# Kernel optimization log

Hardware: AMD Instinct MI355X
Metric: run time of the kernel (lower is better)

The kernel has to match this reference:

```python
import jax, jax.numpy as jnp
import numpy as np

FMAP = 5
C = 2048
NC = 201  # n_classes + 1


def _conv(x, w, stride, pad):
    return jax.lax.conv_general_dilated(
        x, w, (stride, stride), [(pad, pad), (pad, pad)],
        dimension_numbers=('NCHW', 'OIHW', 'NCHW'))


def _bn(x, g, b, eps=1e-5):
    # training-mode batch norm (batch statistics), as in the torch forward
    m = x.mean((0, 2, 3), keepdims=True)
    v = x.var((0, 2, 3), keepdims=True)
    return (x - m) / jnp.sqrt(v + eps) * g[None, :, None, None] + b[None, :, None, None]


def _grid_sample(img, grid):
    # img [B,C,H,W]; grid [B,K,2] normalized coords (x,y), align_corners=True,
    # bilinear, zero padding -> [B,C,K]
    B, Ch, H, W = img.shape
    gx = (grid[..., 0] + 1.0) * 0.5 * (W - 1)
    gy = (grid[..., 1] + 1.0) * 0.5 * (H - 1)
    x0 = jnp.floor(gx); y0 = jnp.floor(gy)
    x1 = x0 + 1.0; y1 = y0 + 1.0
    wx1 = gx - x0; wx0 = 1.0 - wx1
    wy1 = gy - y0; wy0 = 1.0 - wy1
    imgf = img.reshape(B, Ch, H * W)

    def gather(xi, yi):
        valid = (xi >= 0) & (xi <= W - 1) & (yi >= 0) & (yi <= H - 1)
        xi_ = jnp.clip(xi, 0, W - 1).astype(jnp.int32)
        yi_ = jnp.clip(yi, 0, H - 1).astype(jnp.int32)
        idx = yi_ * W + xi_  # [B,K]
        v = jnp.take_along_axis(imgf, idx[:, None, :], axis=2)  # [B,C,K]
        return v * valid[:, None, :].astype(img.dtype)

    out = (gather(x0, y0) * (wx0 * wy0)[:, None, :]
           + gather(x1, y0) * (wx1 * wy0)[:, None, :]
           + gather(x0, y1) * (wx0 * wy1)[:, None, :]
           + gather(x1, y1) * (wx1 * wy1)[:, None, :])
    return out


def setup_inputs() -> dict:
    key = jax.random.key(0)
    ks = jax.random.split(key, 12)
    B = 8
    return {
        'x': jax.random.normal(ks[0], (B, C, 10, 10), jnp.float32),
        'epoch': 1,
        'flag': 0,
        'conv_last_w': jax.random.normal(ks[1], (C, C, 3, 3), jnp.float32) * 0.02,
        'bn_last_g': jnp.ones((C,), jnp.float32),
        'bn_last_b': jnp.zeros((C,), jnp.float32),
        'loc_w1': jax.random.normal(ks[2], (C, C, 3, 3), jnp.float32) * 0.02,
        'loc_g1': jnp.ones((C,), jnp.float32),
        'loc_b1': jnp.zeros((C,), jnp.float32),
        'loc_w2': jax.random.normal(ks[3], (C, C, 3, 3), jnp.float32) * 0.02,
        'loc_g2': jnp.ones((C,), jnp.float32),
        'loc_b2': jnp.zeros((C,), jnp.float32),
        'fc1_w': jax.random.normal(ks[4], (512, C * 9), jnp.float32) * 0.02,
        'fc2_w': jax.random.normal(ks[5], (4, 512), jnp.float32) * 0.001,
        'conv_stn_w': jax.random.normal(ks[6], (NC, C, 3, 3), jnp.float32) * 0.02,
        'conv_stn_b': jnp.zeros((NC,), jnp.float32),
    }


def reference(x, epoch, flag, conv_last_w, bn_last_g, bn_last_b,
              loc_w1, loc_g1, loc_b1, loc_w2, loc_g2, loc_b2,
              fc1_w, fc2_w, conv_stn_w, conv_stn_b):
    B = x.shape[0]
    # backbone tail: conv_last (s=2, pad=1) + bn_last -> [B,2048,5,5]
    f = _bn(_conv(x, conv_last_w, 2, 1), bn_last_g, bn_last_b)

    # localization network (conv-bn-relu x2, pad=1) -> [B,2048,5,5]
    xs = jax.nn.relu(_bn(_conv(f, loc_w1, 1, 1), loc_g1, loc_b1))
    xs = jax.nn.relu(_bn(_conv(xs, loc_w2, 1, 1), loc_g2, loc_b2))
    xs_p = jnp.pad(xs, ((0, 0), (0, 0), (1, 1), (1, 1)))  # [B,2048,7,7]

    # batched per-cell fc_loc: 25 overlapping 3x3 patches (i outer, j inner)
    patches = jnp.stack([xs_p[:, :, i:i + 3, j:j + 3]
                         for i in range(FMAP) for j in range(FMAP)], axis=1)
    patches = patches.reshape(B, FMAP * FMAP, C * 9)  # (C, kh, kw) flatten order
    h = jax.nn.relu(jnp.einsum('bpf,hf->bph', patches, fc1_w))
    p = jnp.einsum('bph,oh->bpo', h, fc2_w)  # [B,25,4]

    # theta = [[1+p0, 0, p1], [0, 1+p2, p3]]
    zero = jnp.zeros_like(p[..., 0])
    row0 = jnp.stack([1.0 + p[..., 0], zero, p[..., 1]], -1)
    row1 = jnp.stack([zero, 1.0 + p[..., 2], p[..., 3]], -1)
    theta = jnp.stack([row0, row1], -2)  # [B,25,2,3]

    # identity affine grid on padded 7x7 map (align_corners=True), 3x3 windows
    lin = jnp.linspace(-1.0, 1.0, FMAP + 2)
    gxm, gym = jnp.meshgrid(lin, lin, indexing='xy')  # gxm[y,x]=lin[x]
    base = jnp.stack([gxm, gym], -1)  # [7,7,2]
    pos = jnp.stack([base[i:i + 3, j:j + 3]
                     for i in range(FMAP) for j in range(FMAP)], 0)
    pos_h = jnp.concatenate([pos.reshape(25, 9, 2), jnp.ones((25, 9, 1))], -1)

    # transformed sampling grids: pos_hom @ theta^T -> [B,25,9,2]
    grids = jnp.einsum('pkc,bpdc->bpkd', pos_h, theta).reshape(B, 25 * 9, 2)

    # batched grid_sample of padded features, then stitch 25 3x3 tiles -> 15x15
    f_p = jnp.pad(f, ((0, 0), (0, 0), (1, 1), (1, 1)))  # [B,2048,7,7]
    samp = _grid_sample(f_p, grids)  # [B,C,225]
    temp = samp.reshape(B, C, FMAP, FMAP, 3, 3).transpose(0, 1, 2, 4, 3, 5)
    temp = temp.reshape(B, C, 3 * FMAP, 3 * FMAP)  # [B,2048,15,15]

    # conv_stn (k=3, s=3) -> [B,201,5,5]; joint softmax over class x position
    out = _conv(temp, conv_stn_w, 3, 0) + conv_stn_b[None, :, None, None]
    s = jax.nn.softmax(out.reshape(B, -1), axis=1).reshape(B, NC, FMAP, FMAP)
    classif_scores = s.sum((2, 3))  # [B,201]
    return classif_scores, s, theta.reshape(B * 25, 2, 3)
```

## Files before the change

kernel.cpp:

```cpp
#include <hip/hip_runtime.h>
#include <hip/hip_bf16.h>


#define GK 18432
#define GN 200
#define NPAD 256

typedef __attribute__((ext_vector_type(8))) short bf16x8;
typedef __attribute__((ext_vector_type(4))) float f32x4;
typedef unsigned int u32;

__global__ __launch_bounds__(256) void im2col_bf16(
    const float* __restrict__ in, __hip_bfloat16* __restrict__ Bt,
    int H, int stride, int pad)
{
    int tid = blockIdx.x * 256 + threadIdx.x;
    int n = tid / GK;
    int k = tid - n * GK;
    float v = 0.f;
    if (n < GN) {
        int c = k / 9; int r9 = k - c * 9;
        int kh = r9 / 3, kw = r9 - kh * 3;
        int b = n / 25; int pp = n - b * 25;
        int oh = pp / 5, ow = pp - oh * 5;
        int r = oh * stride + kh - pad;
        int s = ow * stride + kw - pad;
        if (r >= 0 && r < H && s >= 0 && s < H)
            v = in[(((b * 2048 + c) * H) + r) * H + s];
    }
    Bt[tid] = __float2bfloat16(v);
}

__global__ __launch_bounds__(256) void gridsample_bf16(
    const float* __restrict__ f, const float* __restrict__ gridb,
    __hip_bfloat16* __restrict__ Bt)
{
    int tid = blockIdx.x * 256 + threadIdx.x;
    int n = tid / GK;
    int cq = tid - n * GK;
    float v = 0.f;
    if (n < GN) {
        int c = cq / 9, q = cq - c * 9;
        int b = n / 25, p = n - b * 25;
        int g = (b * 225 + p * 9 + q) * 2;
        float px = gridb[g], py = gridb[g + 1];
        float x0f = floorf(px), y0f = floorf(py);
        int x0 = (int)x0f, y0 = (int)y0f;
        float wx1 = px - x0f, wx0 = 1.f - wx1;
        float wy1 = py - y0f, wy0 = 1.f - wy1;
        const float* fb = f + ((size_t)b * 2048 + c) * 25;
        auto fetch = [&](int xi, int yi) -> float {
            if (xi < 1 || xi > 5 || yi < 1 || yi > 5) return 0.f;
            return fb[(yi - 1) * 5 + (xi - 1)];
        };
        v = fetch(x0, y0) * wx0 * wy0
          + fetch(x0 + 1, y0) * wx1 * wy0
          + fetch(x0, y0 + 1) * wx0 * wy1
          + fetch(x0 + 1, y0 + 1) * wx1 * wy1;
    }
    Bt[tid] = __float2bfloat16(v);
}

__global__ __launch_bounds__(256) void gemm_mfma(
    const float* __restrict__ A, const __hip_bfloat16* __restrict__ Bt,
    float* __restrict__ C, int M, int kchunk)
{
    __shared__ unsigned short As[128 * 40];
    __shared__ unsigned short Bs[128 * 32];

    const int tid = threadIdx.x;
    const int bn = blockIdx.x * 128;
    const int bm = blockIdx.y * 128;
    const int kbase = blockIdx.z * kchunk;

    const int wave = tid >> 6, lane = tid & 63;
    const int wm = (wave & 1) * 64, wn = (wave >> 1) * 64;
    const int lm = lane & 15, lq = lane >> 4;

    const int arow = tid >> 1;
    const int akh = (tid & 1) * 16;
    const bool aok = (bm + arow) < M;
    const float* aptr = A + (size_t)(bm + arow) * GK + kbase + akh;
    uint4* awr = (uint4*)&As[arow * 40 + akh];

    const int brow = wave * 32 + (lane >> 2);
    const int bkoff = (lane & 3) * 8;
    const __hip_bfloat16* bptr0 = Bt + (size_t)(bn + brow) * GK + kbase + bkoff;
    const __hip_bfloat16* bptr1 = bptr0 + (size_t)16 * GK;
    unsigned short* bwr0 = &Bs[wave * 1024];
    unsigned short* bwr1 = &Bs[wave * 1024 + 512];

    f32x4 acc[4][4] = {};

    for (int k0 = 0; k0 < kchunk; k0 += 32) {
        __builtin_amdgcn_global_load_lds((const u32*)(bptr0 + k0), (u32*)bwr0, 16, 0, 0);
        __builtin_amdgcn_global_load_lds((const u32*)(bptr1 + k0), (u32*)bwr1, 16, 0, 0);

        u32 pk[8];
        if (aok) {
            const float4* ap = (const float4*)(aptr + k0);
            float4 a0 = ap[0], a1 = ap[1], a2 = ap[2], a3 = ap[3];
            pk[0] = __builtin_amdgcn_perm(__float_as_uint(a0.y), __float_as_uint(a0.x), 0x07060302u);
            pk[1] = __builtin_amdgcn_perm(__float_as_uint(a0.w), __float_as_uint(a0.z), 0x07060302u);
            pk[2] = __builtin_amdgcn_perm(__float_as_uint(a1.y), __float_as_uint(a1.x), 0x07060302u);
            pk[3] = __builtin_amdgcn_perm(__float_as_uint(a1.w), __float_as_uint(a1.z), 0x07060302u);
            pk[4] = __builtin_amdgcn_perm(__float_as_uint(a2.y), __float_as_uint(a2.x), 0x07060302u);
            pk[5] = __builtin_amdgcn_perm(__float_as_uint(a2.w), __float_as_uint(a2.z), 0x07060302u);
            pk[6] = __builtin_amdgcn_perm(__float_as_uint(a3.y), __float_as_uint(a3.x), 0x07060302u);
            pk[7] = __builtin_amdgcn_perm(__float_as_uint(a3.w), __float_as_uint(a3.z), 0x07060302u);
        } else {
#pragma unroll
            for (int i = 0; i < 8; ++i) pk[i] = 0;
        }
        awr[0] = make_uint4(pk[0], pk[1], pk[2], pk[3]);
        awr[1] = make_uint4(pk[4], pk[5], pk[6], pk[7]);

        __syncthreads();

        bf16x8 af[4], bfr[4];
#pragma unroll
        for (int i = 0; i < 4; ++i) {
            af[i]  = *(const bf16x8*)&As[(wm + i * 16 + lm) * 40 + lq * 8];
            bfr[i] = *(const bf16x8*)&Bs[(wn + i * 16 + lm) * 32 + lq * 8];
        }
#pragma unroll
        for (int i = 0; i < 4; ++i)
#pragma unroll
            for (int j = 0; j < 4; ++j)
                acc[i][j] = __builtin_amdgcn_mfma_f32_16x16x32_bf16(
                    af[i], bfr[j], acc[i][j], 0, 0, 0);

        __syncthreads();
    }

#pragma unroll
    for (int i = 0; i < 4; ++i) {
        int row0 = bm + wm + i * 16 + lq * 4;
#pragma unroll
        for (int j = 0; j < 4; ++j) {
            int col = bn + wn + j * 16 + lm;
            if (col < GN) {
#pragma unroll
                for (int r = 0; r < 4; ++r)
                    if (row0 + r < M)
                        atomicAdd(&C[(size_t)(row0 + r) * GN + col], acc[i][j][r]);
            }
        }
    }
}

__global__ void bnstats_kernel(const float* __restrict__ y,
                               float* __restrict__ meanb,
                               float* __restrict__ rstdb)
{
    int ch = blockIdx.x;
    int lane = threadIdx.x;
    const float* p = y + (size_t)ch * GN;
    float s = 0.f, sq = 0.f;
    for (int idx = lane; idx < GN; idx += 64) {
        float v = p[idx];
        s += v; sq += v * v;
    }
    for (int off = 32; off; off >>= 1) {
        s += __shfl_down(s, off);
        sq += __shfl_down(sq, off);
    }
    if (lane == 0) {
        float m = s * (1.f / 200.f);
        float var = sq * (1.f / 200.f) - m * m;
        meanb[ch] = m;
        rstdb[ch] = rsqrtf(var + 1e-5f);
    }
}

__global__ __launch_bounds__(256) void bn_apply_kernel(
    const float* __restrict__ y, const float* __restrict__ meanb,
    const float* __restrict__ rstdb, const float* __restrict__ g,
    const float* __restrict__ bb, float* __restrict__ out, int relu)
{
    int tid = blockIdx.x * 256 + threadIdx.x;
    if (tid >= 409600) return;
    int b = tid / (2048 * 25);
    int rem = tid % (2048 * 25);
    int c = rem / 25;
    int pp = rem % 25;
    float v = y[(size_t)c * GN + b * 25 + pp];
    v = (v - meanb[c]) * rstdb[c] * g[c] + bb[c];
    if (relu) v = fmaxf(v, 0.f);
    out[tid] = v;
}

__global__ void fc2_kernel(const float* __restrict__ hmat,
                           const float* __restrict__ fc2w,
                           float* __restrict__ pbuf)
{
    int n = blockIdx.x;
    int oo = threadIdx.x >> 6;
    int lane = threadIdx.x & 63;
    float s = 0.f;
#pragma unroll
    for (int j = 0; j < 8; ++j) {
        int hh = lane + 64 * j;
        s += fmaxf(hmat[(size_t)hh * GN + n], 0.f) * fc2w[oo * 512 + hh];
    }
    for (int off = 32; off; off >>= 1) s += __shfl_down(s, off);
    if (lane == 0) pbuf[n * 4 + oo] = s;
}

__global__ void theta_grids_kernel(const float* __restrict__ pbuf,
                                   float* __restrict__ gridb,
                                   float* __restrict__ outT)
{
    int tid = blockIdx.x * 256 + threadIdx.x;
    if (tid >= 1800) return;
    int b = tid / 225;
    int rem = tid % 225;
    int p = rem / 9;
    int k = rem % 9;
    int i = p / 5, j = p % 5;
    int dy = k / 3, dx = k % 3;
    int n = b * 25 + p;
    float p0 = pbuf[n * 4 + 0];
    float p1 = pbuf[n * 4 + 1];
    float p2 = pbuf[n * 4 + 2];
    float p3 = pbuf[n * 4 + 3];
    float x = (float)(j + dx) * (1.f / 3.f) - 1.f;
    float y = (float)(i + dy) * (1.f / 3.f) - 1.f;
    float gx = (1.f + p0) * x + p1;
    float gy = (1.f + p2) * y + p3;
    gridb[tid * 2 + 0] = (gx + 1.f) * 3.f;
    gridb[tid * 2 + 1] = (gy + 1.f) * 3.f;
    if (k == 0) {
        outT[n * 6 + 0] = 1.f + p0;
        outT[n * 6 + 1] = 0.f;
        outT[n * 6 + 2] = p1;
        outT[n * 6 + 3] = 0.f;
        outT[n * 6 + 4] = 1.f + p2;
        outT[n * 6 + 5] = p3;
    }
}

__global__ void softmax_kernel(const float* __restrict__ stn,
                               const float* __restrict__ bias,
                               float* __restrict__ outC,
                               float* __restrict__ outS)
{
    int b = blockIdx.x;
    __shared__ float red[256];
    int t = threadIdx.x;

    float mx = -1e30f;
    for (int idx = t; idx < 5025; idx += 256) {
        int o = idx / 25, pp = idx % 25;
        mx = fmaxf(mx, stn[(size_t)o * GN + b * 25 + pp] + bias[o]);
    }
    red[t] = mx; __syncthreads();
    for (int s = 128; s; s >>= 1) {
        if (t < s) red[t] = fmaxf(red[t], red[t + s]);
        __syncthreads();
    }
    mx = red[0]; __syncthreads();

    float sm = 0.f;
    for (int idx = t; idx < 5025; idx += 256) {
        int o = idx / 25, pp = idx % 25;
        sm += expf(stn[(size_t)o * GN + b * 25 + pp] + bias[o] - mx);
    }
    red[t] = sm; __syncthreads();
    for (int s = 128; s; s >>= 1) {
        if (t < s) red[t] += red[t + s];
        __syncthreads();
    }
    float inv = 1.f / red[0];

    for (int idx = t; idx < 5025; idx += 256) {
        int o = idx / 25, pp = idx % 25;
        outS[b * 5025 + idx] =
            expf(stn[(size_t)o * GN + b * 25 + pp] + bias[o] - mx) * inv;
    }
    for (int o = t; o < 201; o += 256) {
        float cs = 0.f;
        for (int pp = 0; pp < 25; ++pp)
            cs += expf(stn[(size_t)o * GN + b * 25 + pp] + bias[o] - mx);
        outC[b * 201 + o] = cs * inv;
    }
}

extern "C" void kernel_launch(void* const* d_in, const int* in_sizes, int n_in,
                              void* d_out, int out_size, void* d_ws, size_t ws_size,
                              hipStream_t stream)
{
    const float* x           = (const float*)d_in[0];
    const float* conv_last_w = (const float*)d_in[3];
    const float* bn_last_g   = (const float*)d_in[4];
    const float* bn_last_b   = (const float*)d_in[5];
    const float* loc_w1      = (const float*)d_in[6];
    const float* loc_g1      = (const float*)d_in[7];
    const float* loc_b1      = (const float*)d_in[8];
    const float* loc_w2      = (const float*)d_in[9];
    const float* loc_g2      = (const float*)d_in[10];
    const float* loc_b2      = (const float*)d_in[11];
    const float* fc1_w       = (const float*)d_in[12];
    const float* fc2_w       = (const float*)d_in[13];
    const float* conv_stn_w  = (const float*)d_in[14];
    const float* conv_stn_b  = (const float*)d_in[15];

    __hip_bfloat16* Bt = (__hip_bfloat16*)d_ws;
    float* fp    = (float*)((char*)d_ws + (size_t)NPAD * GK * 2);
    float* t1    = fp;
    float* fbuf  = t1 + 409600;
    float* xs1   = fbuf + 409600;
    float* xs    = xs1 + 409600;
    float* hmat  = xs + 409600;
    float* stn   = hmat + 102400;
    float* pbuf  = stn + 40200;
    float* gridb = pbuf + 800;
    float* meanb = gridb + 3600;
    float* rstdb = meanb + 2048;

    float* outC = (float*)d_out;
    float* outS = outC + 8 * 201;
    float* outT = outS + 8 * 201 * 25;

    dim3 b256(256);
    const int nB = (NPAD * GK) / 256;

    im2col_bf16<<<nB, b256, 0, stream>>>(x, Bt, 10, 2, 1);
    hipMemsetAsync(t1, 0, 409600 * sizeof(float), stream);
    gemm_mfma<<<dim3(2, 16, 16), b256, 0, stream>>>(conv_last_w, Bt, t1, 2048, GK / 16);
    bnstats_kernel<<<2048, 64, 0, stream>>>(t1, meanb, rstdb);
    bn_apply_kernel<<<1600, b256, 0, stream>>>(t1, meanb, rstdb, bn_last_g, bn_last_b, fbuf, 0);

    im2col_bf16<<<nB, b256, 0, stream>>>(fbuf, Bt, 5, 1, 1);
    hipMemsetAsync(t1, 0, 409600 * sizeof(float), stream);
    gemm_mfma<<<dim3(2, 16, 16), b256, 0, stream>>>(loc_w1, Bt, t1, 2048, GK / 16);
    bnstats_kernel<<<2048, 64, 0, stream>>>(t1, meanb, rstdb);
    bn_apply_kernel<<<1600, b256, 0, stream>>>(t1, meanb, rstdb, loc_g1, loc_b1, xs1, 1);

    im2col_bf16<<<nB, b256, 0, stream>>>(xs1, Bt, 5, 1, 1);
    hipMemsetAsync(t1, 0, 409600 * sizeof(float), stream);
    gemm_mfma<<<dim3(2, 16, 16), b256, 0, stream>>>(loc_w2, Bt, t1, 2048, GK / 16);
    bnstats_kernel<<<2048, 64, 0, stream>>>(t1, meanb, rstdb);
    bn_apply_kernel<<<1600, b256, 0, stream>>>(t1, meanb, rstdb, loc_g2, loc_b2, xs, 1);

    im2col_bf16<<<nB, b256, 0, stream>>>(xs, Bt, 5, 1, 1);
    hipMemsetAsync(hmat, 0, 102400 * sizeof(float), stream);
    gemm_mfma<<<dim3(2, 4, 32), b256, 0, stream>>>(fc1_w, Bt, hmat, 512, GK / 32);

    fc2_kernel<<<200, 256, 0, stream>>>(hmat, fc2_w, pbuf);
    theta_grids_kernel<<<8, 256, 0, stream>>>(pbuf, gridb, outT);

    gridsample_bf16<<<nB, b256, 0, stream>>>(fbuf, gridb, Bt);

    hipMemsetAsync(stn, 0, 40200 * sizeof(float), stream);
    gemm_mfma<<<dim3(2, 2, 32), b256, 0, stream>>>(conv_stn_w, Bt, stn, 201, GK / 32);

    softmax_kernel<<<8, 256, 0, stream>>>(stn, conv_stn_b, outC, outS);
}
```

Measured before the change: 775.6 us.

## Restructure MFMA GEMM to full-N tiles with double-buffered swizzled B and register-resident A

The GEMM now gives each block all 208 (padded 256) output columns, so the fp32 weight matrix A is read once rather than twice. A rows are loaded straight into registers and converted to bf16 in registers, which removes the A LDS staging. B tiles are double-buffered in LDS with an XOR swizzle and prefetched a step ahead. Split-K is doubled for the smaller GEMMs. This trades more accumulator registers (26 f32x4) and a larger LDS footprint for fewer redundant weight reads and better load/compute overlap.

```diff
diff --git a/kernel.cpp b/kernel.cpp
--- a/kernel.cpp
+++ b/kernel.cpp
@@ -61,89 +61,95 @@
     Bt[tid] = __float2bfloat16(v);
 }
 
-__global__ __launch_bounds__(256) void gemm_mfma(
+__global__ __launch_bounds__(256, 2) void gemm_mfma(
     const float* __restrict__ A, const __hip_bfloat16* __restrict__ Bt,
     float* __restrict__ C, int M, int kchunk)
 {
-    __shared__ unsigned short As[128 * 40];
-    __shared__ unsigned short Bs[128 * 32];
-
-    const int tid = threadIdx.x;
-    const int bn = blockIdx.x * 128;
+    __shared__ unsigned short Bs[2][256 * 32];
+
+    const int tid  = threadIdx.x;
+    const int wave = tid >> 6, lane = tid & 63;
+    const int lm = lane & 15, lq = lane >> 4;
     const int bm = blockIdx.y * 128;
     const int kbase = blockIdx.z * kchunk;
-
-    const int wave = tid >> 6, lane = tid & 63;
-    const int wm = (wave & 1) * 64, wn = (wave >> 1) * 64;
-    const int lm = lane & 15, lq = lane >> 4;
-
-    const int arow = tid >> 1;
-    const int akh = (tid & 1) * 16;
-    const bool aok = (bm + arow) < M;
-    const float* aptr = A + (size_t)(bm + arow) * GK + kbase + akh;
-    uint4* awr = (uint4*)&As[arow * 40 + akh];
-
-    const int brow = wave * 32 + (lane >> 2);
-    const int bkoff = (lane & 3) * 8;
-    const __hip_bfloat16* bptr0 = Bt + (size_t)(bn + brow) * GK + kbase + bkoff;
-    const __hip_bfloat16* bptr1 = bptr0 + (size_t)16 * GK;
-    unsigned short* bwr0 = &Bs[wave * 1024];
-    unsigned short* bwr1 = &Bs[wave * 1024 + 512];
-
-    f32x4 acc[4][4] = {};
-
-    for (int k0 = 0; k0 < kchunk; k0 += 32) {
-        __builtin_amdgcn_global_load_lds((const u32*)(bptr0 + k0), (u32*)bwr0, 16, 0, 0);
-        __builtin_amdgcn_global_load_lds((const u32*)(bptr1 + k0), (u32*)bwr1, 16, 0, 0);
-
-        u32 pk[8];
-        if (aok) {
-            const float4* ap = (const float4*)(aptr + k0);
-            float4 a0 = ap[0], a1 = ap[1], a2 = ap[2], a3 = ap[3];
-            pk[0] = __builtin_amdgcn_perm(__float_as_uint(a0.y), __float_as_uint(a0.x), 0x07060302u);
-            pk[1] = __builtin_amdgcn_perm(__float_as_uint(a0.w), __float_as_uint(a0.z), 0x07060302u);
-            pk[2] = __builtin_amdgcn_perm(__float_as_uint(a1.y), __float_as_uint(a1.x), 0x07060302u);
-            pk[3] = __builtin_amdgcn_perm(__float_as_uint(a1.w), __float_as_uint(a1.z), 0x07060302u);
-            pk[4] = __builtin_amdgcn_perm(__float_as_uint(a2.y), __float_as_uint(a2.x), 0x07060302u);
-            pk[5] = __builtin_amdgcn_perm(__float_as_uint(a2.w), __float_as_uint(a2.z), 0x07060302u);
-            pk[6] = __builtin_amdgcn_perm(__float_as_uint(a3.y), __float_as_uint(a3.x), 0x07060302u);
-            pk[7] = __builtin_amdgcn_perm(__float_as_uint(a3.w), __float_as_uint(a3.z), 0x07060302u);
-        } else {
-#pragma unroll
-            for (int i = 0; i < 8; ++i) pk[i] = 0;
+    const int wm = wave * 32;
+
+    const int koff = (((tid & 3) ^ ((tid >> 3) & 3)) << 3);
+    const __hip_bfloat16* bsrc = Bt + (size_t)(tid >> 2) * GK + kbase + koff;
+    const int xk = lq ^ ((lm >> 1) & 3);
+
+    int r0 = bm + wm + lm;      if (r0 > M - 1) r0 = M - 1;
+    int r1 = bm + wm + 16 + lm; if (r1 > M - 1) r1 = M - 1;
+    const float* ap0 = A + (size_t)r0 * GK + kbase + lq * 8;
+    const float* ap1 = A + (size_t)r1 * GK + kbase + lq * 8;
+
+    f32x4 acc[2][13] = {};
+    const int NS = kchunk >> 5;
+
+    auto stageB = [&](int buf, int k0) {
+        unsigned short* dst = &Bs[buf][tid * 8];
+        const __hip_bfloat16* s = bsrc + k0;
+#pragma unroll
+        for (int r = 0; r < 4; ++r)
+            __builtin_amdgcn_global_load_lds((const u32*)(s + (size_t)r * 64 * GK),
+                                             (u32*)(dst + r * 2048), 16, 0, 0);
+    };
+
+    stageB(0, 0);
+    float4 ar00 = *(const float4*)(ap0 + 0);
+    float4 ar01 = *(const float4*)(ap0 + 4);
+    float4 ar10 = *(const float4*)(ap1 + 0);
+    float4 ar11 = *(const float4*)(ap1 + 4);
+
+    int cur = 0;
+    for (int t = 0; t < NS; ++t) {
+        const int kn = (t + 1 < NS) ? ((t + 1) << 5) : (t << 5);
+        stageB(cur ^ 1, kn);
+        float4 an00 = *(const float4*)(ap0 + kn);
+        float4 an01 = *(const float4*)(ap0 + kn + 4);
+        float4 an10 = *(const float4*)(ap1 + kn);
+        float4 an11 = *(const float4*)(ap1 + kn + 4);
+
+        union { bf16x8 v; u32 u[4]; } af0, af1;
+        af0.u[0] = __builtin_amdgcn_perm(__float_as_uint(ar00.y), __float_as_uint(ar00.x), 0x07060302u);
+        af0.u[1] = __builtin_amdgcn_perm(__float_as_uint(ar00.w), __float_as_uint(ar00.z), 0x07060302u);
+        af0.u[2] = __builtin_amdgcn_perm(__float_as_uint(ar01.y), __float_as_uint(ar01.x), 0x07060302u);
+        af0.u[3] = __builtin_amdgcn_perm(__float_as_uint(ar01.w), __float_as_uint(ar01.z), 0x07060302u);
+        af1.u[0] = __builtin_amdgcn_perm(__float_as_uint(ar10.y), __float_as_uint(ar10.x), 0x07060302u);
+        af1.u[1] = __builtin_amdgcn_perm(__float_as_uint(ar10.w), __float_as_uint(ar10.z), 0x07060302u);
+        af1.u[2] = __builtin_amdgcn_perm(__float_as_uint(ar11.y), __float_as_uint(ar11.x), 0x07060302u);
+        af1.u[3] = __builtin_amdgcn_perm(__float_as_uint(ar11.w), __float_as_uint(ar11.z), 0x07060302u);
+
+        asm volatile("s_waitcnt vmcnt(8)" ::: "memory");
+        __builtin_amdgcn_s_barrier();
+
+#pragma unroll
+        for (int j = 0; j < 13; ++j) {
+            bf16x8 b = *(const bf16x8*)&Bs[cur][(j * 16 + lm) * 32 + xk * 8];
+            acc[0][j] = __builtin_amdgcn_mfma_f32_16x16x32_bf16(af0.v, b, acc[0][j], 0, 0, 0);
+            acc[1][j] = __builtin_amdgcn_mfma_f32_16x16x32_bf16(af1.v, b, acc[1][j], 0, 0, 0);
         }
-        awr[0] = make_uint4(pk[0], pk[1], pk[2], pk[3]);
-        awr[1] = make_uint4(pk[4], pk[5], pk[6], pk[7]);
-
-        __syncthreads();
-
-        bf16x8 af[4], bfr[4];
-#pragma unroll
-        for (int i = 0; i < 4; ++i) {
-            af[i]  = *(const bf16x8*)&As[(wm + i * 16 + lm) * 40 + lq * 8];
-            bfr[i] = *(const bf16x8*)&Bs[(wn + i * 16 + lm) * 32 + lq * 8];
-        }
-#pragma unroll
-        for (int i = 0; i < 4; ++i)
-#pragma unroll
-            for (int j = 0; j < 4; ++j)
-                acc[i][j] = __builtin_amdgcn_mfma_f32_16x16x32_bf16(
-                    af[i], bfr[j], acc[i][j], 0, 0, 0);
-
-        __syncthreads();
-    }
-
-#pragma unroll
-    for (int i = 0; i < 4; ++i) {
+
+        asm volatile("" ::: "memory");
+        __builtin_amdgcn_s_barrier();
+
+        ar00 = an00; ar01 = an01; ar10 = an10; ar11 = an11;
+        cur ^= 1;
+    }
+
+#pragma unroll
+    for (int i = 0; i < 2; ++i) {
         int row0 = bm + wm + i * 16 + lq * 4;
 #pragma unroll
-        for (int j = 0; j < 4; ++j) {
-            int col = bn + wn + j * 16 + lm;
+        for (int j = 0; j < 13; ++j) {
+            int col = j * 16 + lm;
             if (col < GN) {
 #pragma unroll
-                for (int r = 0; r < 4; ++r)
-                    if (row0 + r < M)
-                        atomicAdd(&C[(size_t)(row0 + r) * GN + col], acc[i][j][r]);
+                for (int r = 0; r < 4; ++r) {
+                    int row = row0 + r;
+                    if (row < M)
+                        atomicAdd(&C[(size_t)row * GN + col], acc[i][j][r]);
+                }
             }
         }
     }
@@ -327,25 +333,25 @@
 
     im2col_bf16<<<nB, b256, 0, stream>>>(x, Bt, 10, 2, 1);
     hipMemsetAsync(t1, 0, 409600 * sizeof(float), stream);
-    gemm_mfma<<<dim3(2, 16, 16), b256, 0, stream>>>(conv_last_w, Bt, t1, 2048, GK / 16);
+    gemm_mfma<<<dim3(1, 16, 16), b256, 0, stream>>>(conv_last_w, Bt, t1, 2048, GK / 16);
     bnstats_kernel<<<2048, 64, 0, stream>>>(t1, meanb, rstdb);
     bn_apply_kernel<<<1600, b256, 0, stream>>>(t1, meanb, rstdb, bn_last_g, bn_last_b, fbuf, 0);
 
     im2col_bf16<<<nB, b256, 0, stream>>>(fbuf, Bt, 5, 1, 1);
     hipMemsetAsync(t1, 0, 409600 * sizeof(float), stream);
-    gemm_mfma<<<dim3(2, 16, 16), b256, 0, stream>>>(loc_w1, Bt, t1, 2048, GK / 16);
+    gemm_mfma<<<dim3(1, 16, 16), b256, 0, stream>>>(loc_w1, Bt, t1, 2048, GK / 16);
     bnstats_kernel<<<2048, 64, 0, stream>>>(t1, meanb, rstdb);
     bn_apply_kernel<<<1600, b256, 0, stream>>>(t1, meanb, rstdb, loc_g1, loc_b1, xs1, 1);
 
     im2col_bf16<<<nB, b256, 0, stream>>>(xs1, Bt, 5, 1, 1);
     hipMemsetAsync(t1, 0, 409600 * sizeof(float), stream);
-    gemm_mfma<<<dim3(2, 16, 16), b256, 0, stream>>>(loc_w2, Bt, t1, 2048, GK / 16);
+    gemm_mfma<<<dim3(1, 16, 16), b256, 0, stream>>>(loc_w2, Bt, t1, 2048, GK / 16);
     bnstats_kernel<<<2048, 64, 0, stream>>>(t1, meanb, rstdb);
     bn_apply_kernel<<<1600, b256, 0, stream>>>(t1, meanb, rstdb, loc_g2, loc_b2, xs, 1);
 
     im2col_bf16<<<nB, b256, 0, stream>>>(xs, Bt, 5, 1, 1);
     hipMemsetAsync(hmat, 0, 102400 * sizeof(float), stream);
-    gemm_mfma<<<dim3(2, 4, 32), b256, 0, stream>>>(fc1_w, Bt, hmat, 512, GK / 32);
+    gemm_mfma<<<dim3(1, 4, 64), b256, 0, stream>>>(fc1_w, Bt, hmat, 512, GK / 64);
 
     fc2_kernel<<<200, 256, 0, stream>>>(hmat, fc2_w, pbuf);
     theta_grids_kernel<<<8, 256, 0, stream>>>(pbuf, gridb, outT);
@@ -353,7 +359,7 @@
     gridsample_bf16<<<nB, b256, 0, stream>>>(fbuf, gridb, Bt);
 
     hipMemsetAsync(stn, 0, 40200 * sizeof(float), stream);
-    gemm_mfma<<<dim3(2, 2, 32), b256, 0, stream>>>(conv_stn_w, Bt, stn, 201, GK / 32);
+    gemm_mfma<<<dim3(1, 2, 64), b256, 0, stream>>>(conv_stn_w, Bt, stn, 201, GK / 64);
 
     softmax_kernel<<<8, 256, 0, stream>>>(stn, conv_stn_b, outC, outS);
 }
```

Measured after the change: 761.1 us. About the same (-1.9%).
